# Performance work log

Hardware: AMD Instinct MI355X
Metric: run time of the kernel (lower is better)

The kernel has to match this reference:

```python
import jax, jax.numpy as jnp
import numpy as np

LEAKY_SLOPE = 0.01  # torch nn.LeakyReLU / F.leaky_relu default


def gcn_diffusion(adj, order, feat):
    # A_gcn = adj + I; sym-normalized diffusion D^-1/2 A D^-1/2 applied repeatedly
    B, N, _ = adj.shape
    A = adj + jnp.eye(N, dtype=adj.dtype)
    dinv_sqrt = jnp.sum(A, axis=2) ** -0.5  # [B, N]
    outs = []
    h = feat
    for _ in range(order):
        h = jnp.matmul(A, dinv_sqrt[..., None] * h) * dinv_sqrt[..., None]
        outs.append(h)
    return outs


def scattering_s4(adj, feat):
    # lazy random walk P = 1/2 (I + A D^-1); wavelets Psi_j = P^{2^{j-1}} - P^{2^j}
    dinv = 1.0 / jnp.sum(adj, axis=2)  # [B, N]
    p = feat
    us = []
    for _ in range(8):  # powers P^1 .. P^8
        p = 0.5 * p + 0.5 * jnp.matmul(adj, dinv[..., None] * p)
        us.append(p)
    h1 = feat - us[0]      # I - P
    h2 = us[0] - us[1]     # P - P^2
    h3 = us[1] - us[3]     # P^2 - P^4
    h4 = us[3] - us[7]     # P^4 - P^8
    return h1, h2, h3, h4


def sctconv(X, adj, W1, b1, W2, b2, a, moment):
    leaky = lambda x: jax.nn.leaky_relu(x, LEAKY_SLOPE)
    h = X  # [B, N, F]
    hA, hA2, hA3 = gcn_diffusion(adj, 3, X)
    hA, hA2, hA3 = leaky(hA), leaky(hA2), leaky(hA3)
    s1, s2, s3, s4 = scattering_s4(adj, X)
    mom = jnp.asarray(moment, dtype=X.dtype)
    s1 = jnp.abs(s1) ** mom
    s2 = jnp.abs(s2) ** mom
    s3 = jnp.abs(s3) ** mom
    s4 = jnp.abs(s4) ** mom
    # NOTE: original concatenates only (hA, hA2, s1..s4) -> 6 branches; hA3 is unused.
    h_all = jnp.stack([hA, hA2, s1, s2, s3, s4], axis=1)  # [B, 6, N, F]
    h_b = jnp.broadcast_to(h[:, None], h_all.shape)        # [B, 6, N, F]
    a_input = jnp.concatenate([h_b, h_all], axis=3)        # [B, 6, N, 2F]
    e = jnp.einsum('bknc,c->bkn', jax.nn.relu(a_input), a[:, 0])  # [B, 6, N]
    attention = jax.nn.softmax(e, axis=1)[..., None]       # [B, 6, N, 1]
    h_prime = jnp.mean(attention * h_all, axis=1)          # [B, N, F]
    out = leaky(h_prime @ W1.T + b1)
    out = leaky(out @ W2.T + b2)
    return out


def setup_inputs() -> dict:
    key = jax.random.key(0)
    kx, ka, k1, k2, k3, k4, k5 = jax.random.split(key, 7)
    B, N, F = 8, 4096, 64
    X = jax.random.normal(kx, (B, N, F), dtype=jnp.float32)
    adj = jax.random.uniform(ka, (B, N, N), dtype=jnp.float32)
    s = 1.0 / np.sqrt(F)
    W1 = jax.random.uniform(k1, (F, F), minval=-s, maxval=s, dtype=jnp.float32)
    b1 = jax.random.uniform(k2, (F,), minval=-s, maxval=s, dtype=jnp.float32)
    W2 = jax.random.uniform(k3, (F, F), minval=-s, maxval=s, dtype=jnp.float32)
    b2 = jax.random.uniform(k4, (F,), minval=-s, maxval=s, dtype=jnp.float32)
    a = jax.random.normal(k5, (2 * F, 1), dtype=jnp.float32) * 0.1
    return {"X": X, "adj": adj, "W1": W1, "b1": b1, "W2": W2, "b2": b2, "a": a, "moment": 1}


def reference(X, adj, W1, b1, W2, b2, a, moment):
    return sctconv(X, adj, W1, b1, W2, b2, a, moment)
```

## Files before the change

kernel.cpp:

```cpp
#include <hip/hip_runtime.h>
#include <hip/hip_bf16.h>
#include <cstdio>
#include <cstdint>

#define BB 8
#define NN 4096
#define FF 64

typedef __attribute__((ext_vector_type(8))) short bf16x8;
typedef __attribute__((ext_vector_type(4))) float f32x4;

__device__ __forceinline__ unsigned short f2bf(float f){
  unsigned int u = __float_as_uint(f);
  u += 0x7FFFu + ((u >> 16) & 1u);
  return (unsigned short)(u >> 16);
}

__device__ __forceinline__ float leaky01(float x){ return x > 0.f ? x : 0.01f * x; }


__global__ __launch_bounds__(256) void k_convert(const float* __restrict__ adj,
    unsigned short* __restrict__ At, float* __restrict__ dinv, float* __restrict__ dsq)
{
  const int bid = blockIdx.x;
  const int b = bid & 7, mt = bid >> 3, m0 = mt * 32;
  const int tid = threadIdx.x;
  const int r = tid >> 3, g = tid & 7;
  const float* src = adj + ((size_t)b * NN + m0 + r) * NN + ((g ^ (r & 7)) << 3);
  unsigned short* dst = At + (size_t)bid * 64 * 2048 + (tid << 3);
  float s = 0.f;
  for (int t = 0; t < 64; ++t){
    const float* p = src + t * 64;
    float4 a = *(const float4*)p;
    float4 c = *(const float4*)(p + 4);
    s += ((a.x + a.y) + (a.z + a.w)) + ((c.x + c.y) + (c.z + c.w));
    bf16x8 v;
    v[0] = (short)f2bf(a.x); v[1] = (short)f2bf(a.y); v[2] = (short)f2bf(a.z); v[3] = (short)f2bf(a.w);
    v[4] = (short)f2bf(c.x); v[5] = (short)f2bf(c.y); v[6] = (short)f2bf(c.z); v[7] = (short)f2bf(c.w);
    *(bf16x8*)(dst + (size_t)t * 2048) = v;
  }
  s += __shfl_xor(s, 1); s += __shfl_xor(s, 2); s += __shfl_xor(s, 4);
  if (g == 0){
    dinv[(size_t)b * NN + m0 + r] = 1.0f / s;
    dsq [(size_t)b * NN + m0 + r] = 1.0f / sqrtf(s + 1.0f);
  }
}

__global__ __launch_bounds__(256) void k_prep(const float* __restrict__ X,
    const float* __restrict__ dinv, const float* __restrict__ dsq,
    unsigned short* __restrict__ Bt)
{
  const int b = blockIdx.y, n0 = blockIdx.x * 64, tid = threadIdx.x;
  __shared__ unsigned short tg[64][68], ts[64][68];
  #pragma unroll
  for (int i = 0; i < 4; ++i){
    int idx = i * 256 + tid, n = idx >> 4, c4 = (idx & 15) * 4;
    size_t rb = (size_t)b * NN + n0 + n;
    float4 x = *(const float4*)(X + rb * 64 + c4);
    float di = dinv[b * NN + n0 + n], dv = dsq[b * NN + n0 + n];
    tg[c4 + 0][n] = f2bf(dv * x.x); tg[c4 + 1][n] = f2bf(dv * x.y);
    tg[c4 + 2][n] = f2bf(dv * x.z); tg[c4 + 3][n] = f2bf(dv * x.w);
    ts[c4 + 0][n] = f2bf(di * x.x); ts[c4 + 1][n] = f2bf(di * x.y);
    ts[c4 + 2][n] = f2bf(di * x.z); ts[c4 + 3][n] = f2bf(di * x.w);
  }
  __syncthreads();
  const int t = n0 >> 6;
  #pragma unroll
  for (int it = 0; it < 8; ++it){
    int idx = it * 256 + tid;
    int half = idx & 1, l = (idx >> 1) & 63, kk = (idx >> 7) & 1, ct = (idx >> 8) & 7;
    int cl = ((ct & 3) << 4) + (l & 15);
    int nl = kk * 32 + ((l >> 4) << 3) + half * 4;
    ushort4 v = (ct < 4) ? *(const ushort4*)&tg[cl][nl] : *(const ushort4*)&ts[cl][nl];
    *(ushort4*)(Bt + ((((size_t)b * 8 + ct) * 64 + t) * 2 + kk) * 512 + (l << 3) + half * 4) = v;
  }
}

template<int NC>
__global__ __launch_bounds__(256, 4) void k_gemm_fused(
    const unsigned short* __restrict__ At,
    const unsigned short* __restrict__ BtR, int ct0,
    const float* __restrict__ sprev, float* __restrict__ P, float* __restrict__ snap,
    const float* __restrict__ dinv, int writeVtS,
    const float* __restrict__ gprev, float* __restrict__ gout,
    const float* __restrict__ dsq, int writeVtG,
    unsigned short* __restrict__ BtW)
{
  constexpr int NF = NC / 64;
  __shared__ __align__(16) unsigned short As[4][32 * 64];
  const int bid = blockIdx.x;
  const int b = bid & 7, mt = bid >> 3, m0 = mt * 32;
  const int tid = threadIdx.x;
  const int w = tid >> 6, l = tid & 63;
  const int r0 = l & 15, hq = l >> 4, sw = r0 & 7;
  const unsigned short* Atile = At + (size_t)bid * 131072;
  const unsigned short* Bb[NF];
  #pragma unroll
  for (int ni = 0; ni < NF; ++ni)
    Bb[ni] = BtR + (((size_t)b * 8 + ct0 + w * NF + ni) * 64) * 1024 + (l << 3);

  auto stageA = [&](int buf, int t){
    const unsigned short* gp = Atile + (size_t)t * 2048 + (tid << 3);
    __builtin_amdgcn_global_load_lds((const __attribute__((address_space(1))) void*)gp,
        (__attribute__((address_space(3))) void*)(&As[buf][tid << 3]), 16, 0, 0);
  };
  auto LDB = [&](bf16x8 (&pb)[NF][2], int t){
    #pragma unroll
    for (int ni = 0; ni < NF; ++ni)
      #pragma unroll
      for (int kk = 0; kk < 2; ++kk)
        pb[ni][kk] = *(const bf16x8*)(Bb[ni] + (size_t)t * 1024 + kk * 512);
  };

  bf16x8 b0[NF][2], b1[NF][2];
  f32x4 acc[2][NF];
  #pragma unroll
  for (int mi = 0; mi < 2; ++mi)
    #pragma unroll
    for (int ni = 0; ni < NF; ++ni)
      #pragma unroll
      for (int j = 0; j < 4; ++j) acc[mi][ni][j] = 0.f;

  stageA(0, 0); stageA(1, 1); stageA(2, 2);
  LDB(b0, 0);

  #define SUBSTEP(T, BCUR, BNXT)                                                  \
    do {                                                                          \
      const int _t = (T);                                                         \
      __builtin_amdgcn_s_barrier();                                               \
      asm volatile("" ::: "memory");                                              \
      const bool _st = (_t + 3 < 64);                                             \
      if (_st) stageA((_t + 3) & 3, _t + 3);                                      \
      if (_t + 1 < 64) LDB(BNXT, _t + 1);                                         \
      if (_t >= 61){ asm volatile("s_waitcnt vmcnt(0)" ::: "memory"); }           \
      else if constexpr (NC == 128){ asm volatile("s_waitcnt vmcnt(5)" ::: "memory"); } \
      else { asm volatile("s_waitcnt vmcnt(3)" ::: "memory"); }                   \
      asm volatile("" ::: "memory");                                              \
      _Pragma("unroll")                                                           \
      for (int kk = 0; kk < 2; ++kk){                                             \
        const int g8 = ((kk * 4 + hq) ^ sw) << 3;                                 \
        bf16x8 af0 = *(const bf16x8*)&As[_t & 3][(r0) * 64 + g8];                 \
        bf16x8 af1 = *(const bf16x8*)&As[_t & 3][(16 + r0) * 64 + g8];            \
        _Pragma("unroll")                                                         \
        for (int ni = 0; ni < NF; ++ni){                                          \
          acc[0][ni] = __builtin_amdgcn_mfma_f32_16x16x32_bf16(af0, BCUR[ni][kk], acc[0][ni], 0, 0, 0); \
          acc[1][ni] = __builtin_amdgcn_mfma_f32_16x16x32_bf16(af1, BCUR[ni][kk], acc[1][ni], 0, 0, 0); \
        }                                                                         \
      }                                                                           \
      asm volatile("" ::: "memory");                                              \
    } while (0)

  #pragma unroll 1
  for (int t = 0; t < 64; t += 2){
    SUBSTEP(t,     b0, b1);
    SUBSTEP(t + 1, b1, b0);
  }
  #undef SUBSTEP

  const bool isScat = (NC == 64) || (w >= 2);
  if (isScat){
    const int wS = (NC == 64) ? w : (w - 2);
    #pragma unroll
    for (int mi = 0; mi < 2; ++mi){
      const int rb = m0 + mi * 16 + hq * 4;
      const size_t rowb = (size_t)b * NN + rb;
      float4 dv4 = *(const float4*)(dinv + (size_t)b * NN + rb);
      #pragma unroll
      for (int ni = 0; ni < NF; ++ni){
        const int cs = wS * 16 * NF + ni * 16 + r0;
        float pn[4];
        #pragma unroll
        for (int j = 0; j < 4; ++j){
          float pv = sprev[(rowb + j) * 64 + cs];
          pn[j] = 0.5f * (pv + acc[mi][ni][j]);
          P[(rowb + j) * 64 + cs] = pn[j];
        }
        if (snap){
          #pragma unroll
          for (int j = 0; j < 4; ++j) snap[(rowb + j) * 64 + cs] = pn[j];
        }
        if (writeVtS){
          const int ct = 4 + wS * NF + ni;
          const int tp = rb >> 6, kkp = (rb >> 5) & 1;
          const int lp = r0 + 16 * ((rb >> 3) & 3), hf = (rb >> 2) & 1;
          ushort4 vv = make_ushort4(f2bf(dv4.x * pn[0]), f2bf(dv4.y * pn[1]),
                                    f2bf(dv4.z * pn[2]), f2bf(dv4.w * pn[3]));
          *(ushort4*)(BtW + ((((size_t)b * 8 + ct) * 64 + tp) * 2 + kkp) * 512
                          + (lp << 3) + hf * 4) = vv;
        }
      }
    }
  }
  if constexpr (NC == 128){
    if (!isScat){
      #pragma unroll
      for (int mi = 0; mi < 2; ++mi){
        const int rb = m0 + mi * 16 + hq * 4;
        const size_t rowb = (size_t)b * NN + rb;
        float4 dq4 = *(const float4*)(dsq + (size_t)b * NN + rb);
        #pragma unroll
        for (int ni = 0; ni < NF; ++ni){
          const int cg = w * 16 * NF + ni * 16 + r0;
          float hn[4];
          const float dq[4] = {dq4.x, dq4.y, dq4.z, dq4.w};
          #pragma unroll
          for (int j = 0; j < 4; ++j){
            float hv = gprev[(rowb + j) * 64 + cg];
            hn[j] = (acc[mi][ni][j] + dq[j] * hv) * dq[j];
            gout[(rowb + j) * 64 + cg] = hn[j];
          }
          if (writeVtG){
            const int ct = w * NF + ni;
            const int tp = rb >> 6, kkp = (rb >> 5) & 1;
            const int lp = r0 + 16 * ((rb >> 3) & 3), hf = (rb >> 2) & 1;
            ushort4 vv = make_ushort4(f2bf(dq[0] * hn[0]), f2bf(dq[1] * hn[1]),
                                      f2bf(dq[2] * hn[2]), f2bf(dq[3] * hn[3]));
            *(ushort4*)(BtW + ((((size_t)b * 8 + ct) * 64 + tp) * 2 + kkp) * 512
                            + (lp << 3) + hf * 4) = vv;
          }
        }
      }
    }
  }
}

__global__ __launch_bounds__(256) void k_attn(
    const float* __restrict__ X,  const float* __restrict__ hA, const float* __restrict__ hA2,
    const float* __restrict__ U1, const float* __restrict__ U2, const float* __restrict__ U4,
    const float* __restrict__ U8, const float* __restrict__ W1, const float* __restrict__ b1,
    const float* __restrict__ W2, const float* __restrict__ b2, const float* __restrict__ av,
    const int* __restrict__ momp, float* __restrict__ out)
{
  __shared__ float W1s[64][65], W2s[64][65];
  __shared__ float a1s[64], a2s[64], b1s[64], b2s[64];
  __shared__ float hp[4][64], o1[4][64];
  const int tid = threadIdx.x;
  for (int e = tid; e < 4096; e += 256){
    W1s[e >> 6][e & 63] = W1[e];
    W2s[e >> 6][e & 63] = W2[e];
  }
  if (tid < 64){ a1s[tid] = av[tid]; a2s[tid] = av[64 + tid]; b1s[tid] = b1[tid]; b2s[tid] = b2[tid]; }
  __syncthreads();
  const int w = tid >> 6, l = tid & 63;
  size_t row = (size_t)blockIdx.x * 4 + w;
  size_t off = row * 64 + l;
  float x  = X[off];
  float u1 = U1[off], u2 = U2[off], u4 = U4[off], u8 = U8[off];
  float br[6];
  br[0] = leaky01(hA[off]);
  br[1] = leaky01(hA2[off]);
  float d1 = fabsf(x - u1), d2 = fabsf(u1 - u2), d3 = fabsf(u2 - u4), d4 = fabsf(u4 - u8);
  int mom = *momp;
  if (mom == 1){ br[2] = d1; br[3] = d2; br[4] = d3; br[5] = d4; }
  else {
    float m = (float)mom;
    br[2] = powf(d1, m); br[3] = powf(d2, m); br[4] = powf(d3, m); br[5] = powf(d4, m);
  }
  float v = fmaxf(x, 0.f) * a1s[l];
  for (int o = 32; o; o >>= 1) v += __shfl_xor(v, o);
  float base = v;
  float e[6];
  #pragma unroll
  for (int k = 0; k < 6; ++k){
    float t = fmaxf(br[k], 0.f) * a2s[l];
    for (int o = 32; o; o >>= 1) t += __shfl_xor(t, o);
    e[k] = base + t;
  }
  float mx = e[0];
  #pragma unroll
  for (int k = 1; k < 6; ++k) mx = fmaxf(mx, e[k]);
  float s = 0.f, att[6];
  #pragma unroll
  for (int k = 0; k < 6; ++k){ att[k] = expf(e[k] - mx); s += att[k]; }
  float inv = 1.0f / (6.0f * s);
  float hpv = 0.f;
  #pragma unroll
  for (int k = 0; k < 6; ++k) hpv += att[k] * br[k];
  hpv *= inv;
  hp[w][l] = hpv;
  __syncthreads();
  float acc = b1s[l];
  #pragma unroll 8
  for (int c = 0; c < 64; ++c) acc += hp[w][c] * W1s[l][c];
  o1[w][l] = leaky01(acc);
  __syncthreads();
  float acc2 = b2s[l];
  #pragma unroll 8
  for (int c = 0; c < 64; ++c) acc2 += o1[w][c] * W2s[l][c];
  out[off] = leaky01(acc2);
}

static constexpr size_t OFF_ADJB = 0;
static constexpr size_t OFF_VTA  = OFF_ADJB + (size_t)BB * NN * NN * 2;
static constexpr size_t OFF_VTB  = OFF_VTA  + (size_t)BB * 128 * NN * 2;
static constexpr size_t OFF_HA   = OFF_VTB  + (size_t)BB * 128 * NN * 2;
static constexpr size_t OFF_HA2  = OFF_HA   + (size_t)BB * NN * 64 * 4;
static constexpr size_t OFF_P    = OFF_HA2  + (size_t)BB * NN * 64 * 4;
static constexpr size_t OFF_U1   = OFF_P    + (size_t)BB * NN * 64 * 4;
static constexpr size_t OFF_U2   = OFF_U1   + (size_t)BB * NN * 64 * 4;
static constexpr size_t OFF_U4   = OFF_U2   + (size_t)BB * NN * 64 * 4;
static constexpr size_t OFF_U8   = OFF_U4   + (size_t)BB * NN * 64 * 4;
static constexpr size_t OFF_DINV = OFF_U8   + (size_t)BB * NN * 64 * 4;
static constexpr size_t OFF_DS   = OFF_DINV + (size_t)BB * NN * 4;
static constexpr size_t WS_NEED  = OFF_DS   + (size_t)BB * NN * 4;

extern "C" void kernel_launch(void* const* d_in, const int* in_sizes, int n_in,
                              void* d_out, int out_size, void* d_ws, size_t ws_size,
                              hipStream_t stream)
{
  const float* X   = (const float*)d_in[0];
  const float* adj = (const float*)d_in[1];
  const float* W1  = (const float*)d_in[2];
  const float* b1  = (const float*)d_in[3];
  const float* W2  = (const float*)d_in[4];
  const float* b2  = (const float*)d_in[5];
  const float* av  = (const float*)d_in[6];
  const int*  momp = (const int*)d_in[7];
  float* out = (float*)d_out;

  if (ws_size < WS_NEED){
    fprintf(stderr, "kernel_launch: workspace too small: %zu < %zu\n", ws_size, WS_NEED);
    return;
  }
  char* w = (char*)d_ws;
  unsigned short* At  = (unsigned short*)(w + OFF_ADJB);
  unsigned short* vtA = (unsigned short*)(w + OFF_VTA);
  unsigned short* vtB = (unsigned short*)(w + OFF_VTB);
  float* hA   = (float*)(w + OFF_HA);
  float* hA2  = (float*)(w + OFF_HA2);
  float* P    = (float*)(w + OFF_P);
  float* U1   = (float*)(w + OFF_U1);
  float* U2   = (float*)(w + OFF_U2);
  float* U4   = (float*)(w + OFF_U4);
  float* U8   = (float*)(w + OFF_U8);
  float* dinv = (float*)(w + OFF_DINV);
  float* dsq  = (float*)(w + OFF_DS);

  k_convert<<<1024, 256, 0, stream>>>(adj, At, dinv, dsq);
  dim3 tg64(NN / 64, BB);
  k_prep<<<tg64, 256, 0, stream>>>(X, dinv, dsq, vtA);

  k_gemm_fused<128><<<1024, 256, 0, stream>>>(At, vtA, 0,
      X, P, U1, dinv, 1, X, hA, dsq, 1, vtB);
  k_gemm_fused<128><<<1024, 256, 0, stream>>>(At, vtB, 0,
      P, P, U2, dinv, 1, hA, hA2, dsq, 0, vtA);
  unsigned short* vr = vtA;
  unsigned short* vw = vtB;
  for (int k = 3; k <= 8; ++k){
    float* snap = (k == 4) ? U4 : nullptr;
    float* pdst = (k == 8) ? U8 : P;
    k_gemm_fused<64><<<1024, 256, 0, stream>>>(At, vr, 4,
        P, pdst, snap, dinv, (k < 8) ? 1 : 0, nullptr, nullptr, nullptr, 0, vw);
    unsigned short* t = vr; vr = vw; vw = t;
  }

  k_attn<<<BB * NN / 4, 256, 0, stream>>>(X, hA, hA2, U1, U2, U4, U8,
                                          W1, b1, W2, b2, av, momp, out);
}
```

Measured before the change: 784.9 us.

## Deepen GEMM software pipeline with five LDS stages and B prefetch two ahead

```diff
diff --git a/kernel.cpp b/kernel.cpp
--- a/kernel.cpp
+++ b/kernel.cpp
@@ -87,7 +87,8 @@
     unsigned short* __restrict__ BtW)
 {
   constexpr int NF = NC / 64;
-  __shared__ __align__(16) unsigned short As[4][32 * 64];
+  constexpr int BAHEAD = (NC == 64) ? 2 : 1;
+  __shared__ __align__(16) unsigned short As[5][32 * 64];
   const int bid = blockIdx.x;
   const int b = bid & 7, mt = bid >> 3, m0 = mt * 32;
   const int tid = threadIdx.x;
@@ -112,7 +113,6 @@
         pb[ni][kk] = *(const bf16x8*)(Bb[ni] + (size_t)t * 1024 + kk * 512);
   };
 
-  bf16x8 b0[NF][2], b1[NF][2];
   f32x4 acc[2][NF];
   #pragma unroll
   for (int mi = 0; mi < 2; ++mi)
@@ -121,41 +121,72 @@
       #pragma unroll
       for (int j = 0; j < 4; ++j) acc[mi][ni][j] = 0.f;
 
-  stageA(0, 0); stageA(1, 1); stageA(2, 2);
-  LDB(b0, 0);
-
-  #define SUBSTEP(T, BCUR, BNXT)                                                  \
-    do {                                                                          \
-      const int _t = (T);                                                         \
-      __builtin_amdgcn_s_barrier();                                               \
-      asm volatile("" ::: "memory");                                              \
-      const bool _st = (_t + 3 < 64);                                             \
-      if (_st) stageA((_t + 3) & 3, _t + 3);                                      \
-      if (_t + 1 < 64) LDB(BNXT, _t + 1);                                         \
-      if (_t >= 61){ asm volatile("s_waitcnt vmcnt(0)" ::: "memory"); }           \
-      else if constexpr (NC == 128){ asm volatile("s_waitcnt vmcnt(5)" ::: "memory"); } \
-      else { asm volatile("s_waitcnt vmcnt(3)" ::: "memory"); }                   \
-      asm volatile("" ::: "memory");                                              \
-      _Pragma("unroll")                                                           \
-      for (int kk = 0; kk < 2; ++kk){                                             \
-        const int g8 = ((kk * 4 + hq) ^ sw) << 3;                                 \
-        bf16x8 af0 = *(const bf16x8*)&As[_t & 3][(r0) * 64 + g8];                 \
-        bf16x8 af1 = *(const bf16x8*)&As[_t & 3][(16 + r0) * 64 + g8];            \
-        _Pragma("unroll")                                                         \
-        for (int ni = 0; ni < NF; ++ni){                                          \
-          acc[0][ni] = __builtin_amdgcn_mfma_f32_16x16x32_bf16(af0, BCUR[ni][kk], acc[0][ni], 0, 0, 0); \
-          acc[1][ni] = __builtin_amdgcn_mfma_f32_16x16x32_bf16(af1, BCUR[ni][kk], acc[1][ni], 0, 0, 0); \
-        }                                                                         \
-      }                                                                           \
-      asm volatile("" ::: "memory");                                              \
-    } while (0)
-
-  #pragma unroll 1
-  for (int t = 0; t < 64; t += 2){
-    SUBSTEP(t,     b0, b1);
-    SUBSTEP(t + 1, b1, b0);
-  }
-  #undef SUBSTEP
+  auto COMPUTE = [&](int ibuf, bf16x8 (&pb)[NF][2]){
+    const unsigned short* asb = &As[ibuf][0];
+    #pragma unroll
+    for (int kk = 0; kk < 2; ++kk){
+      const int g8 = ((kk * 4 + hq) ^ sw) << 3;
+      bf16x8 af0 = *(const bf16x8*)&asb[(r0) * 64 + g8];
+      bf16x8 af1 = *(const bf16x8*)&asb[(16 + r0) * 64 + g8];
+      #pragma unroll
+      for (int ni = 0; ni < NF; ++ni){
+        acc[0][ni] = __builtin_amdgcn_mfma_f32_16x16x32_bf16(af0, pb[ni][kk], acc[0][ni], 0, 0, 0);
+        acc[1][ni] = __builtin_amdgcn_mfma_f32_16x16x32_bf16(af1, pb[ni][kk], acc[1][ni], 0, 0, 0);
+      }
+    }
+  };
+
+  bf16x8 b0[NF][2], b1[NF][2], b2[NF][2], b3[NF][2];
+  int ibc = 0, ibs = 3;
+
+  #define SUB(T, BCUR, BLD, VM) do {                                            \
+    if ((T) + BAHEAD < 64) LDB(BLD, (T) + BAHEAD);                              \
+    if ((T) + 3 < 64){ stageA(ibs, (T) + 3); ibs = (ibs == 4) ? 0 : ibs + 1; }  \
+    asm volatile("s_waitcnt vmcnt(" #VM ")" ::: "memory");                      \
+    __builtin_amdgcn_s_barrier();                                               \
+    asm volatile("" ::: "memory");                                              \
+    COMPUTE(ibc, BCUR); ibc = (ibc == 4) ? 0 : ibc + 1;                         \
+    asm volatile("" ::: "memory");                                              \
+  } while (0)
+
+  if constexpr (NC == 64){
+    LDB(b0, 0); LDB(b1, 1);
+    stageA(0, 0); stageA(1, 1); stageA(2, 2);
+    SUB(0, b0, b2, 5);
+    SUB(1, b1, b3, 7);
+    SUB(2, b2, b0, 7);
+    SUB(3, b3, b1, 7);
+    #pragma unroll 1
+    for (int tb = 4; tb < 60; tb += 4){
+      SUB(tb + 0, b0, b2, 7);
+      SUB(tb + 1, b1, b3, 7);
+      SUB(tb + 2, b2, b0, 7);
+      SUB(tb + 3, b3, b1, 7);
+    }
+    SUB(60, b0, b2, 7);
+    SUB(61, b1, b3, 6);
+    SUB(62, b2, b0, 3);
+    SUB(63, b3, b1, 0);
+  } else {
+    LDB(b0, 0);
+    stageA(0, 0); stageA(1, 1); stageA(2, 2);
+    SUB(0, b0, b1, 7);
+    SUB(1, b1, b0, 6);
+    SUB(2, b0, b1, 6);
+    SUB(3, b1, b0, 6);
+    #pragma unroll 1
+    for (int tb = 4; tb < 60; tb += 4){
+      SUB(tb + 0, b0, b1, 6);
+      SUB(tb + 1, b1, b0, 6);
+      SUB(tb + 2, b0, b1, 6);
+      SUB(tb + 3, b1, b0, 6);
+    }
+    SUB(60, b0, b1, 6);
+    SUB(61, b1, b0, 5);
+    SUB(62, b0, b1, 4);
+    SUB(63, b1, b0, 0);
+  }
+  #undef SUB
 
   const bool isScat = (NC == 64) || (w >= 2);
   if (isScat){
```

Result: no change. 782.8 us (-0.3%).

## Double GEMM row tile to 64 rows and restructure prefetch pipeline

Applied to the files above, without the earlier changes.

```diff
diff --git a/kernel.cpp b/kernel.cpp
--- a/kernel.cpp
+++ b/kernel.cpp
@@ -23,26 +23,37 @@
     unsigned short* __restrict__ At, float* __restrict__ dinv, float* __restrict__ dsq)
 {
   const int bid = blockIdx.x;
-  const int b = bid & 7, mt = bid >> 3, m0 = mt * 32;
+  const int b = bid & 7, mt = bid >> 3, m0 = mt * 64;
   const int tid = threadIdx.x;
   const int r = tid >> 3, g = tid & 7;
-  const float* src = adj + ((size_t)b * NN + m0 + r) * NN + ((g ^ (r & 7)) << 3);
-  unsigned short* dst = At + (size_t)bid * 64 * 2048 + (tid << 3);
-  float s = 0.f;
+  const float* src0 = adj + ((size_t)b * NN + m0 + r) * NN + ((g ^ (r & 7)) << 3);
+  const float* src1 = src0 + (size_t)32 * NN;
+  unsigned short* dst0 = At + (size_t)bid * 262144 + (((r)      * 8 + g) << 3);
+  unsigned short* dst1 = At + (size_t)bid * 262144 + (((r + 32) * 8 + g) << 3);
+  float s0 = 0.f, s1 = 0.f;
   for (int t = 0; t < 64; ++t){
-    const float* p = src + t * 64;
-    float4 a = *(const float4*)p;
-    float4 c = *(const float4*)(p + 4);
-    s += ((a.x + a.y) + (a.z + a.w)) + ((c.x + c.y) + (c.z + c.w));
+    const float* p0 = src0 + t * 64;
+    float4 a = *(const float4*)p0, c = *(const float4*)(p0 + 4);
+    s0 += ((a.x + a.y) + (a.z + a.w)) + ((c.x + c.y) + (c.z + c.w));
     bf16x8 v;
-    v[0] = (short)f2bf(a.x); v[1] = (short)f2bf(a.y); v[2] = (short)f2bf(a.z); v[3] = (short)f2bf(a.w);
-    v[4] = (short)f2bf(c.x); v[5] = (short)f2bf(c.y); v[6] = (short)f2bf(c.z); v[7] = (short)f2bf(c.w);
-    *(bf16x8*)(dst + (size_t)t * 2048) = v;
-  }
-  s += __shfl_xor(s, 1); s += __shfl_xor(s, 2); s += __shfl_xor(s, 4);
+    v[0]=(short)f2bf(a.x); v[1]=(short)f2bf(a.y); v[2]=(short)f2bf(a.z); v[3]=(short)f2bf(a.w);
+    v[4]=(short)f2bf(c.x); v[5]=(short)f2bf(c.y); v[6]=(short)f2bf(c.z); v[7]=(short)f2bf(c.w);
+    *(bf16x8*)(dst0 + (size_t)t * 4096) = v;
+    const float* p1 = src1 + t * 64;
+    float4 e = *(const float4*)p1, h = *(const float4*)(p1 + 4);
+    s1 += ((e.x + e.y) + (e.z + e.w)) + ((h.x + h.y) + (h.z + h.w));
+    bf16x8 u;
+    u[0]=(short)f2bf(e.x); u[1]=(short)f2bf(e.y); u[2]=(short)f2bf(e.z); u[3]=(short)f2bf(e.w);
+    u[4]=(short)f2bf(h.x); u[5]=(short)f2bf(h.y); u[6]=(short)f2bf(h.z); u[7]=(short)f2bf(h.w);
+    *(bf16x8*)(dst1 + (size_t)t * 4096) = u;
+  }
+  s0 += __shfl_xor(s0, 1); s0 += __shfl_xor(s0, 2); s0 += __shfl_xor(s0, 4);
+  s1 += __shfl_xor(s1, 1); s1 += __shfl_xor(s1, 2); s1 += __shfl_xor(s1, 4);
   if (g == 0){
-    dinv[(size_t)b * NN + m0 + r] = 1.0f / s;
-    dsq [(size_t)b * NN + m0 + r] = 1.0f / sqrtf(s + 1.0f);
+    dinv[(size_t)b * NN + m0 + r] = 1.0f / s0;
+    dsq [(size_t)b * NN + m0 + r] = 1.0f / sqrtf(s0 + 1.0f);
+    dinv[(size_t)b * NN + m0 + 32 + r] = 1.0f / s1;
+    dsq [(size_t)b * NN + m0 + 32 + r] = 1.0f / sqrtf(s1 + 1.0f);
   }
 }
 
@@ -77,7 +88,7 @@
 }
 
 template<int NC>
-__global__ __launch_bounds__(256, 4) void k_gemm_fused(
+__global__ __launch_bounds__(256, 2) void k_gemm_fused(
     const unsigned short* __restrict__ At,
     const unsigned short* __restrict__ BtR, int ct0,
     const float* __restrict__ sprev, float* __restrict__ P, float* __restrict__ snap,
@@ -87,81 +98,104 @@
     unsigned short* __restrict__ BtW)
 {
   constexpr int NF = NC / 64;
-  __shared__ __align__(16) unsigned short As[4][32 * 64];
+  __shared__ __align__(16) unsigned short As[4][64 * 64];
   const int bid = blockIdx.x;
-  const int b = bid & 7, mt = bid >> 3, m0 = mt * 32;
+  const int b = bid & 7, mt = bid >> 3, m0 = mt * 64;
   const int tid = threadIdx.x;
   const int w = tid >> 6, l = tid & 63;
   const int r0 = l & 15, hq = l >> 4, sw = r0 & 7;
-  const unsigned short* Atile = At + (size_t)bid * 131072;
-  const unsigned short* Bb[NF];
-  #pragma unroll
-  for (int ni = 0; ni < NF; ++ni)
-    Bb[ni] = BtR + (((size_t)b * 8 + ct0 + w * NF + ni) * 64) * 1024 + (l << 3);
+  const unsigned short* Atile = At + (size_t)bid * 262144;
+  const unsigned short* Bb0 = BtR + (((size_t)b * 8 + ct0 + w * NF) * 64) * 1024 + (l << 3);
+  const unsigned short* Bb1 = Bb0 + (size_t)64 * 1024;
 
   auto stageA = [&](int buf, int t){
-    const unsigned short* gp = Atile + (size_t)t * 2048 + (tid << 3);
-    __builtin_amdgcn_global_load_lds((const __attribute__((address_space(1))) void*)gp,
+    const unsigned short* gp0 = Atile + (size_t)t * 4096 + (tid << 3);
+    __builtin_amdgcn_global_load_lds((const __attribute__((address_space(1))) void*)gp0,
         (__attribute__((address_space(3))) void*)(&As[buf][tid << 3]), 16, 0, 0);
+    __builtin_amdgcn_global_load_lds((const __attribute__((address_space(1))) void*)(gp0 + 2048),
+        (__attribute__((address_space(3))) void*)(&As[buf][(256 + tid) << 3]), 16, 0, 0);
   };
-  auto LDB = [&](bf16x8 (&pb)[NF][2], int t){
-    #pragma unroll
-    for (int ni = 0; ni < NF; ++ni)
-      #pragma unroll
-      for (int kk = 0; kk < 2; ++kk)
-        pb[ni][kk] = *(const bf16x8*)(Bb[ni] + (size_t)t * 1024 + kk * 512);
-  };
-
-  bf16x8 b0[NF][2], b1[NF][2];
-  f32x4 acc[2][NF];
-  #pragma unroll
-  for (int mi = 0; mi < 2; ++mi)
+
+  f32x4 acc[4][NF];
+  #pragma unroll
+  for (int mi = 0; mi < 4; ++mi)
     #pragma unroll
     for (int ni = 0; ni < NF; ++ni)
       #pragma unroll
       for (int j = 0; j < 4; ++j) acc[mi][ni][j] = 0.f;
 
-  stageA(0, 0); stageA(1, 1); stageA(2, 2);
-  LDB(b0, 0);
-
-  #define SUBSTEP(T, BCUR, BNXT)                                                  \
-    do {                                                                          \
-      const int _t = (T);                                                         \
-      __builtin_amdgcn_s_barrier();                                               \
-      asm volatile("" ::: "memory");                                              \
-      const bool _st = (_t + 3 < 64);                                             \
-      if (_st) stageA((_t + 3) & 3, _t + 3);                                      \
-      if (_t + 1 < 64) LDB(BNXT, _t + 1);                                         \
-      if (_t >= 61){ asm volatile("s_waitcnt vmcnt(0)" ::: "memory"); }           \
-      else if constexpr (NC == 128){ asm volatile("s_waitcnt vmcnt(5)" ::: "memory"); } \
-      else { asm volatile("s_waitcnt vmcnt(3)" ::: "memory"); }                   \
-      asm volatile("" ::: "memory");                                              \
-      _Pragma("unroll")                                                           \
-      for (int kk = 0; kk < 2; ++kk){                                             \
-        const int g8 = ((kk * 4 + hq) ^ sw) << 3;                                 \
-        bf16x8 af0 = *(const bf16x8*)&As[_t & 3][(r0) * 64 + g8];                 \
-        bf16x8 af1 = *(const bf16x8*)&As[_t & 3][(16 + r0) * 64 + g8];            \
-        _Pragma("unroll")                                                         \
-        for (int ni = 0; ni < NF; ++ni){                                          \
-          acc[0][ni] = __builtin_amdgcn_mfma_f32_16x16x32_bf16(af0, BCUR[ni][kk], acc[0][ni], 0, 0, 0); \
-          acc[1][ni] = __builtin_amdgcn_mfma_f32_16x16x32_bf16(af1, BCUR[ni][kk], acc[1][ni], 0, 0, 0); \
-        }                                                                         \
-      }                                                                           \
-      asm volatile("" ::: "memory");                                              \
-    } while (0)
-
-  #pragma unroll 1
-  for (int t = 0; t < 64; t += 2){
-    SUBSTEP(t,     b0, b1);
-    SUBSTEP(t + 1, b1, b0);
-  }
-  #undef SUBSTEP
+  #define VMW(N) asm volatile("s_waitcnt vmcnt(" #N ")" ::: "memory")
+  #define BARX do{ __builtin_amdgcn_s_barrier(); asm volatile("" ::: "memory"); }while(0)
+
+  if constexpr (NC == 64){
+    bf16x8 b0[2], b1[2], b2[2], b3[2];
+    #define LDB1(PB, T) do{ \
+      PB[0] = *(const bf16x8*)(Bb0 + (size_t)(T) * 1024); \
+      PB[1] = *(const bf16x8*)(Bb0 + (size_t)(T) * 1024 + 512); }while(0)
+    #define CMP64(IB, PB) do{ \
+      const unsigned short* asb = &As[(IB)][0]; \
+      _Pragma("unroll") for (int kk = 0; kk < 2; ++kk){ \
+        const int g8 = ((kk * 4 + hq) ^ sw) << 3; \
+        _Pragma("unroll") for (int mi = 0; mi < 4; ++mi){ \
+          bf16x8 af = *(const bf16x8*)&asb[(mi * 16 + r0) * 64 + g8]; \
+          acc[mi][0] = __builtin_amdgcn_mfma_f32_16x16x32_bf16(af, PB[kk], acc[mi][0], 0, 0, 0); \
+        } } }while(0)
+    #define SUB64(T, BC, BL, N) do{ \
+      if ((T) + 2 < 64){ LDB1(BL, (T) + 2); stageA(((T) + 2) & 3, (T) + 2); } \
+      VMW(N); BARX; CMP64((T) & 3, BC); asm volatile("" ::: "memory"); }while(0)
+
+    stageA(0, 0); stageA(1, 1);
+    LDB1(b0, 0); LDB1(b1, 1);
+    SUB64(0, b0, b2, 6);
+    SUB64(1, b1, b3, 8);
+    #pragma unroll 1
+    for (int T0 = 2; T0 <= 58; T0 += 4){
+      SUB64(T0 + 0, b2, b0, 8);
+      SUB64(T0 + 1, b3, b1, 8);
+      SUB64(T0 + 2, b0, b2, 8);
+      SUB64(T0 + 3, b1, b3, 8);
+    }
+    SUB64(62, b2, b0, 4);
+    SUB64(63, b3, b1, 0);
+  } else {
+    bf16x8 b0[2][2], b1[2][2];
+    #define LDB2(PB, T) do{ \
+      PB[0][0] = *(const bf16x8*)(Bb0 + (size_t)(T) * 1024); \
+      PB[0][1] = *(const bf16x8*)(Bb0 + (size_t)(T) * 1024 + 512); \
+      PB[1][0] = *(const bf16x8*)(Bb1 + (size_t)(T) * 1024); \
+      PB[1][1] = *(const bf16x8*)(Bb1 + (size_t)(T) * 1024 + 512); }while(0)
+    #define CMP128(IB, PB) do{ \
+      const unsigned short* asb = &As[(IB)][0]; \
+      _Pragma("unroll") for (int kk = 0; kk < 2; ++kk){ \
+        const int g8 = ((kk * 4 + hq) ^ sw) << 3; \
+        _Pragma("unroll") for (int mi = 0; mi < 4; ++mi){ \
+          bf16x8 af = *(const bf16x8*)&asb[(mi * 16 + r0) * 64 + g8]; \
+          acc[mi][0] = __builtin_amdgcn_mfma_f32_16x16x32_bf16(af, PB[0][kk], acc[mi][0], 0, 0, 0); \
+          acc[mi][1] = __builtin_amdgcn_mfma_f32_16x16x32_bf16(af, PB[1][kk], acc[mi][1], 0, 0, 0); \
+        } } }while(0)
+    #define SUB128(T, BC, BL, N) do{ \
+      if ((T) + 1 < 64) LDB2(BL, (T) + 1); \
+      if ((T) + 2 < 64) stageA(((T) + 2) & 3, (T) + 2); \
+      VMW(N); BARX; CMP128((T) & 3, BC); asm volatile("" ::: "memory"); }while(0)
+
+    stageA(0, 0); stageA(1, 1);
+    LDB2(b0, 0);
+    SUB128(0, b0, b1, 6);
+    #pragma unroll 1
+    for (int T0 = 1; T0 <= 59; T0 += 2){
+      SUB128(T0 + 0, b1, b0, 8);
+      SUB128(T0 + 1, b0, b1, 8);
+    }
+    SUB128(61, b1, b0, 8);
+    SUB128(62, b0, b1, 6);
+    SUB128(63, b1, b0, 0);
+  }
 
   const bool isScat = (NC == 64) || (w >= 2);
   if (isScat){
     const int wS = (NC == 64) ? w : (w - 2);
     #pragma unroll
-    for (int mi = 0; mi < 2; ++mi){
+    for (int mi = 0; mi < 4; ++mi){
       const int rb = m0 + mi * 16 + hq * 4;
       const size_t rowb = (size_t)b * NN + rb;
       float4 dv4 = *(const float4*)(dinv + (size_t)b * NN + rb);
@@ -194,7 +228,7 @@
   if constexpr (NC == 128){
     if (!isScat){
       #pragma unroll
-      for (int mi = 0; mi < 2; ++mi){
+      for (int mi = 0; mi < 4; ++mi){
         const int rb = m0 + mi * 16 + hq * 4;
         const size_t rowb = (size_t)b * NN + rb;
         float4 dq4 = *(const float4*)(dsq + (size_t)b * NN + rb);
@@ -336,20 +370,20 @@
   float* dinv = (float*)(w + OFF_DINV);
   float* dsq  = (float*)(w + OFF_DS);
 
-  k_convert<<<1024, 256, 0, stream>>>(adj, At, dinv, dsq);
+  k_convert<<<512, 256, 0, stream>>>(adj, At, dinv, dsq);
   dim3 tg64(NN / 64, BB);
   k_prep<<<tg64, 256, 0, stream>>>(X, dinv, dsq, vtA);
 
-  k_gemm_fused<128><<<1024, 256, 0, stream>>>(At, vtA, 0,
+  k_gemm_fused<128><<<512, 256, 0, stream>>>(At, vtA, 0,
       X, P, U1, dinv, 1, X, hA, dsq, 1, vtB);
-  k_gemm_fused<128><<<1024, 256, 0, stream>>>(At, vtB, 0,
+  k_gemm_fused<128><<<512, 256, 0, stream>>>(At, vtB, 0,
       P, P, U2, dinv, 1, hA, hA2, dsq, 0, vtA);
   unsigned short* vr = vtA;
   unsigned short* vw = vtB;
   for (int k = 3; k <= 8; ++k){
     float* snap = (k == 4) ? U4 : nullptr;
     float* pdst = (k == 8) ? U8 : P;
-    k_gemm_fused<64><<<1024, 256, 0, stream>>>(At, vr, 4,
+    k_gemm_fused<64><<<512, 256, 0, stream>>>(At, vr, 4,
         P, pdst, snap, dinv, (k < 8) ? 1 : 0, nullptr, nullptr, nullptr, 0, vw);
     unsigned short* t = vr; vr = vw; vw = t;
   }
```

Result: faster. 696.7 us (-11.2%).

## Enlarge GEMM row tile to 128 with B staged in LDS and 512-thread blocks

Applied to the files above, without the earlier changes.

```diff
diff --git a/kernel.cpp b/kernel.cpp
--- a/kernel.cpp
+++ b/kernel.cpp
@@ -23,26 +23,40 @@
     unsigned short* __restrict__ At, float* __restrict__ dinv, float* __restrict__ dsq)
 {
   const int bid = blockIdx.x;
-  const int b = bid & 7, mt = bid >> 3, m0 = mt * 32;
+  const int b = bid & 7, mt = bid >> 3, m0 = mt * 128;
   const int tid = threadIdx.x;
   const int r = tid >> 3, g = tid & 7;
-  const float* src = adj + ((size_t)b * NN + m0 + r) * NN + ((g ^ (r & 7)) << 3);
-  unsigned short* dst = At + (size_t)bid * 64 * 2048 + (tid << 3);
-  float s = 0.f;
+  const float* src[4];
+  unsigned short* dst[4];
+  float s[4];
+  #pragma unroll
+  for (int q = 0; q < 4; ++q){
+    const int row = r + q * 32;
+    src[q] = adj + ((size_t)b * NN + m0 + row) * NN + ((g ^ (r & 7)) << 3);
+    dst[q] = At + (size_t)bid * 524288 + ((row * 8 + g) << 3);
+    s[q] = 0.f;
+  }
   for (int t = 0; t < 64; ++t){
-    const float* p = src + t * 64;
-    float4 a = *(const float4*)p;
-    float4 c = *(const float4*)(p + 4);
-    s += ((a.x + a.y) + (a.z + a.w)) + ((c.x + c.y) + (c.z + c.w));
-    bf16x8 v;
-    v[0] = (short)f2bf(a.x); v[1] = (short)f2bf(a.y); v[2] = (short)f2bf(a.z); v[3] = (short)f2bf(a.w);
-    v[4] = (short)f2bf(c.x); v[5] = (short)f2bf(c.y); v[6] = (short)f2bf(c.z); v[7] = (short)f2bf(c.w);
-    *(bf16x8*)(dst + (size_t)t * 2048) = v;
-  }
-  s += __shfl_xor(s, 1); s += __shfl_xor(s, 2); s += __shfl_xor(s, 4);
-  if (g == 0){
-    dinv[(size_t)b * NN + m0 + r] = 1.0f / s;
-    dsq [(size_t)b * NN + m0 + r] = 1.0f / sqrtf(s + 1.0f);
+    #pragma unroll
+    for (int q = 0; q < 4; ++q){
+      const float* p = src[q] + t * 64;
+      float4 a = *(const float4*)p, c = *(const float4*)(p + 4);
+      s[q] += ((a.x + a.y) + (a.z + a.w)) + ((c.x + c.y) + (c.z + c.w));
+      bf16x8 v;
+      v[0]=(short)f2bf(a.x); v[1]=(short)f2bf(a.y); v[2]=(short)f2bf(a.z); v[3]=(short)f2bf(a.w);
+      v[4]=(short)f2bf(c.x); v[5]=(short)f2bf(c.y); v[6]=(short)f2bf(c.z); v[7]=(short)f2bf(c.w);
+      *(bf16x8*)(dst[q] + (size_t)t * 8192) = v;
+    }
+  }
+  #pragma unroll
+  for (int q = 0; q < 4; ++q){
+    float sv = s[q];
+    sv += __shfl_xor(sv, 1); sv += __shfl_xor(sv, 2); sv += __shfl_xor(sv, 4);
+    if (g == 0){
+      const int row = m0 + r + q * 32;
+      dinv[(size_t)b * NN + row] = 1.0f / sv;
+      dsq [(size_t)b * NN + row] = 1.0f / sqrtf(sv + 1.0f);
+    }
   }
 }
 
@@ -77,7 +91,7 @@
 }
 
 template<int NC>
-__global__ __launch_bounds__(256, 4) void k_gemm_fused(
+__global__ __launch_bounds__(512, 1) void k_gemm_fused(
     const unsigned short* __restrict__ At,
     const unsigned short* __restrict__ BtR, int ct0,
     const float* __restrict__ sprev, float* __restrict__ P, float* __restrict__ snap,
@@ -87,87 +101,94 @@
     unsigned short* __restrict__ BtW)
 {
   constexpr int NF = NC / 64;
-  __shared__ __align__(16) unsigned short As[4][32 * 64];
+  __shared__ __align__(16) unsigned short As[4][128 * 64];
+  __shared__ __align__(16) unsigned short Bs[4][NF * 4 * 1024];
   const int bid = blockIdx.x;
-  const int b = bid & 7, mt = bid >> 3, m0 = mt * 32;
+  const int b = bid & 7, mt = bid >> 3, m0 = mt * 128;
   const int tid = threadIdx.x;
   const int w = tid >> 6, l = tid & 63;
+  const int wh = w >> 2, wc = w & 3;
   const int r0 = l & 15, hq = l >> 4, sw = r0 & 7;
-  const unsigned short* Atile = At + (size_t)bid * 131072;
-  const unsigned short* Bb[NF];
-  #pragma unroll
-  for (int ni = 0; ni < NF; ++ni)
-    Bb[ni] = BtR + (((size_t)b * 8 + ct0 + w * NF + ni) * 64) * 1024 + (l << 3);
+  const unsigned short* Atile = At + (size_t)bid * 524288;
 
   auto stageA = [&](int buf, int t){
-    const unsigned short* gp = Atile + (size_t)t * 2048 + (tid << 3);
-    __builtin_amdgcn_global_load_lds((const __attribute__((address_space(1))) void*)gp,
-        (__attribute__((address_space(3))) void*)(&As[buf][tid << 3]), 16, 0, 0);
+    #pragma unroll
+    for (int i = 0; i < 2; ++i){
+      const int idx = i * 512 + tid;
+      const unsigned short* gp = Atile + (size_t)t * 8192 + (idx << 3);
+      __builtin_amdgcn_global_load_lds((const __attribute__((address_space(1))) void*)gp,
+          (__attribute__((address_space(3))) void*)(&As[buf][idx << 3]), 16, 0, 0);
+    }
   };
-  auto LDB = [&](bf16x8 (&pb)[NF][2], int t){
+  auto stageB = [&](int buf, int t){
+    #pragma unroll
+    for (int i = 0; i < NF; ++i){
+      const int idx = i * 512 + tid;
+      const int ctl = idx >> 7, e = (idx & 127) << 3;
+      const unsigned short* gp = BtR + (((size_t)b * 8 + ct0 + ctl) * 64 + t) * 1024 + e;
+      __builtin_amdgcn_global_load_lds((const __attribute__((address_space(1))) void*)gp,
+          (__attribute__((address_space(3))) void*)(&Bs[buf][idx << 3]), 16, 0, 0);
+    }
+  };
+
+  f32x4 acc[4][NF];
+  #pragma unroll
+  for (int mi = 0; mi < 4; ++mi)
     #pragma unroll
     for (int ni = 0; ni < NF; ++ni)
       #pragma unroll
-      for (int kk = 0; kk < 2; ++kk)
-        pb[ni][kk] = *(const bf16x8*)(Bb[ni] + (size_t)t * 1024 + kk * 512);
+      for (int j = 0; j < 4; ++j) acc[mi][ni][j] = 0.f;
+
+  auto CMP = [&](int ib){
+    const unsigned short* asb = &As[ib][0];
+    const unsigned short* bsb = &Bs[ib][0];
+    #pragma unroll
+    for (int kk = 0; kk < 2; ++kk){
+      const int g8 = ((kk * 4 + hq) ^ sw) << 3;
+      bf16x8 pb[NF];
+      #pragma unroll
+      for (int ni = 0; ni < NF; ++ni)
+        pb[ni] = *(const bf16x8*)&bsb[(wc * NF + ni) * 1024 + kk * 512 + (l << 3)];
+      #pragma unroll
+      for (int mi = 0; mi < 4; ++mi){
+        bf16x8 af = *(const bf16x8*)&asb[(wh * 64 + mi * 16 + r0) * 64 + g8];
+        #pragma unroll
+        for (int ni = 0; ni < NF; ++ni)
+          acc[mi][ni] = __builtin_amdgcn_mfma_f32_16x16x32_bf16(af, pb[ni], acc[mi][ni], 0, 0, 0);
+      }
+    }
   };
 
-  bf16x8 b0[NF][2], b1[NF][2];
-  f32x4 acc[2][NF];
-  #pragma unroll
-  for (int mi = 0; mi < 2; ++mi)
-    #pragma unroll
-    for (int ni = 0; ni < NF; ++ni)
-      #pragma unroll
-      for (int j = 0; j < 4; ++j) acc[mi][ni][j] = 0.f;
-
-  stageA(0, 0); stageA(1, 1); stageA(2, 2);
-  LDB(b0, 0);
-
-  #define SUBSTEP(T, BCUR, BNXT)                                                  \
-    do {                                                                          \
-      const int _t = (T);                                                         \
-      __builtin_amdgcn_s_barrier();                                               \
-      asm volatile("" ::: "memory");                                              \
-      const bool _st = (_t + 3 < 64);                                             \
-      if (_st) stageA((_t + 3) & 3, _t + 3);                                      \
-      if (_t + 1 < 64) LDB(BNXT, _t + 1);                                         \
-      if (_t >= 61){ asm volatile("s_waitcnt vmcnt(0)" ::: "memory"); }           \
-      else if constexpr (NC == 128){ asm volatile("s_waitcnt vmcnt(5)" ::: "memory"); } \
-      else { asm volatile("s_waitcnt vmcnt(3)" ::: "memory"); }                   \
-      asm volatile("" ::: "memory");                                              \
-      _Pragma("unroll")                                                           \
-      for (int kk = 0; kk < 2; ++kk){                                             \
-        const int g8 = ((kk * 4 + hq) ^ sw) << 3;                                 \
-        bf16x8 af0 = *(const bf16x8*)&As[_t & 3][(r0) * 64 + g8];                 \
-        bf16x8 af1 = *(const bf16x8*)&As[_t & 3][(16 + r0) * 64 + g8];            \
-        _Pragma("unroll")                                                         \
-        for (int ni = 0; ni < NF; ++ni){                                          \
-          acc[0][ni] = __builtin_amdgcn_mfma_f32_16x16x32_bf16(af0, BCUR[ni][kk], acc[0][ni], 0, 0, 0); \
-          acc[1][ni] = __builtin_amdgcn_mfma_f32_16x16x32_bf16(af1, BCUR[ni][kk], acc[1][ni], 0, 0, 0); \
-        }                                                                         \
-      }                                                                           \
-      asm volatile("" ::: "memory");                                              \
-    } while (0)
-
-  #pragma unroll 1
-  for (int t = 0; t < 64; t += 2){
-    SUBSTEP(t,     b0, b1);
-    SUBSTEP(t + 1, b1, b0);
-  }
-  #undef SUBSTEP
-
-  const bool isScat = (NC == 64) || (w >= 2);
+  #define VMW(N) asm volatile("s_waitcnt vmcnt(" #N ")" ::: "memory")
+  #define BARX do{ __builtin_amdgcn_s_barrier(); asm volatile("" ::: "memory"); }while(0)
+  #define SUB(T, N) do{ \
+    if ((T) + 2 < 64){ stageA(((T)+2)&3, (T)+2); stageB(((T)+2)&3, (T)+2); } \
+    VMW(N); BARX; CMP((T)&3); asm volatile("" ::: "memory"); }while(0)
+
+  stageA(0, 0); stageB(0, 0); stageA(1, 1); stageB(1, 1);
+  if constexpr (NC == 64){
+    SUB(0, 6);
+    #pragma unroll 1
+    for (int t = 1; t < 62; ++t) SUB(t, 6);
+    SUB(62, 3); SUB(63, 0);
+  } else {
+    SUB(0, 8);
+    #pragma unroll 1
+    for (int t = 1; t < 62; ++t) SUB(t, 8);
+    SUB(62, 4); SUB(63, 0);
+  }
+  #undef SUB
+
+  const bool isScat = (NC == 64) || (wc >= 2);
   if (isScat){
-    const int wS = (NC == 64) ? w : (w - 2);
-    #pragma unroll
-    for (int mi = 0; mi < 2; ++mi){
-      const int rb = m0 + mi * 16 + hq * 4;
+    #pragma unroll
+    for (int mi = 0; mi < 4; ++mi){
+      const int rb = m0 + wh * 64 + mi * 16 + hq * 4;
       const size_t rowb = (size_t)b * NN + rb;
       float4 dv4 = *(const float4*)(dinv + (size_t)b * NN + rb);
       #pragma unroll
       for (int ni = 0; ni < NF; ++ni){
-        const int cs = wS * 16 * NF + ni * 16 + r0;
+        const int cs = (NC == 64) ? (wc * 16 + r0) : ((wc - 2) * 32 + ni * 16 + r0);
         float pn[4];
         #pragma unroll
         for (int j = 0; j < 4; ++j){
@@ -180,7 +201,7 @@
           for (int j = 0; j < 4; ++j) snap[(rowb + j) * 64 + cs] = pn[j];
         }
         if (writeVtS){
-          const int ct = 4 + wS * NF + ni;
+          const int ct = (NC == 64) ? (4 + wc) : (4 + (wc - 2) * 2 + ni);
           const int tp = rb >> 6, kkp = (rb >> 5) & 1;
           const int lp = r0 + 16 * ((rb >> 3) & 3), hf = (rb >> 2) & 1;
           ushort4 vv = make_ushort4(f2bf(dv4.x * pn[0]), f2bf(dv4.y * pn[1]),
@@ -194,13 +215,13 @@
   if constexpr (NC == 128){
     if (!isScat){
       #pragma unroll
-      for (int mi = 0; mi < 2; ++mi){
-        const int rb = m0 + mi * 16 + hq * 4;
+      for (int mi = 0; mi < 4; ++mi){
+        const int rb = m0 + wh * 64 + mi * 16 + hq * 4;
         const size_t rowb = (size_t)b * NN + rb;
         float4 dq4 = *(const float4*)(dsq + (size_t)b * NN + rb);
         #pragma unroll
         for (int ni = 0; ni < NF; ++ni){
-          const int cg = w * 16 * NF + ni * 16 + r0;
+          const int cg = wc * 32 + ni * 16 + r0;
           float hn[4];
           const float dq[4] = {dq4.x, dq4.y, dq4.z, dq4.w};
           #pragma unroll
@@ -210,7 +231,7 @@
             gout[(rowb + j) * 64 + cg] = hn[j];
           }
           if (writeVtG){
-            const int ct = w * NF + ni;
+            const int ct = wc * 2 + ni;
             const int tp = rb >> 6, kkp = (rb >> 5) & 1;
             const int lp = r0 + 16 * ((rb >> 3) & 3), hf = (rb >> 2) & 1;
             ushort4 vv = make_ushort4(f2bf(dq[0] * hn[0]), f2bf(dq[1] * hn[1]),
@@ -336,20 +357,20 @@
   float* dinv = (float*)(w + OFF_DINV);
   float* dsq  = (float*)(w + OFF_DS);
 
-  k_convert<<<1024, 256, 0, stream>>>(adj, At, dinv, dsq);
+  k_convert<<<256, 256, 0, stream>>>(adj, At, dinv, dsq);
   dim3 tg64(NN / 64, BB);
   k_prep<<<tg64, 256, 0, stream>>>(X, dinv, dsq, vtA);
 
-  k_gemm_fused<128><<<1024, 256, 0, stream>>>(At, vtA, 0,
+  k_gemm_fused<128><<<256, 512, 0, stream>>>(At, vtA, 0,
       X, P, U1, dinv, 1, X, hA, dsq, 1, vtB);
-  k_gemm_fused<128><<<1024, 256, 0, stream>>>(At, vtB, 0,
+  k_gemm_fused<128><<<256, 512, 0, stream>>>(At, vtB, 0,
       P, P, U2, dinv, 1, hA, hA2, dsq, 0, vtA);
   unsigned short* vr = vtA;
   unsigned short* vw = vtB;
   for (int k = 3; k <= 8; ++k){
     float* snap = (k == 4) ? U4 : nullptr;
     float* pdst = (k == 8) ? U8 : P;
-    k_gemm_fused<64><<<1024, 256, 0, stream>>>(At, vr, 4,
+    k_gemm_fused<64><<<256, 512, 0, stream>>>(At, vr, 4,
         P, pdst, snap, dinv, (k < 8) ? 1 : 0, nullptr, nullptr, nullptr, 0, vw);
     unsigned short* t = vr; vr = vw; vw = t;
   }
```

New measurement: 778.4 us. Within noise of the previous version (-0.8%).
